# Performance work log

Measured on AMD Instinct MI355X. Metric: run time of the kernel, lower is better.

## Reference

```python
import jax, jax.numpy as jnp
import numpy as np

N_NODES = 50000
N_EDGES = 800000
NF = 128
HC = 128
NC = 40


def sage_conv(x, src, dst, Wl, Wr, b, num_nodes):
    """PyG SAGEConv with mean aggregation:
    out = lin_l(mean_{j in N(i)} x_j) + lin_r(x_i), bias folded into lin_l."""
    msgs = x[src]                                             # [E, F] gather
    agg = jax.ops.segment_sum(msgs, dst, num_segments=num_nodes)  # [N, F]
    cnt = jax.ops.segment_sum(jnp.ones((src.shape[0],), dtype=x.dtype), dst,
                              num_segments=num_nodes)          # [N]
    mean = agg / jnp.clip(cnt, 1.0)[:, None]                   # mean aggregation
    return mean @ Wl.T + x @ Wr.T + b


def setup_inputs() -> dict:
    key = jax.random.key(0)
    k = jax.random.split(key, 8)
    x = jax.random.normal(k[0], (N_NODES, NF), dtype=jnp.float32)
    edge_index = jax.random.randint(k[1], (2, N_EDGES), 0, N_NODES, dtype=jnp.int32)
    s1 = 1.0 / np.sqrt(NF)
    s2 = 1.0 / np.sqrt(HC)
    Wl1 = jax.random.uniform(k[2], (HC, NF), jnp.float32, -s1, s1)
    Wr1 = jax.random.uniform(k[3], (HC, NF), jnp.float32, -s1, s1)
    b1 = jnp.zeros((HC,), jnp.float32)
    Wl2 = jax.random.uniform(k[4], (NC, HC), jnp.float32, -s2, s2)
    Wr2 = jax.random.uniform(k[5], (NC, HC), jnp.float32, -s2, s2)
    b2 = jnp.zeros((NC,), jnp.float32)
    return {"x": x, "edge_index": edge_index, "Wl1": Wl1, "Wr1": Wr1,
            "b1": b1, "Wl2": Wl2, "Wr2": Wr2, "b2": b2}


def reference(x, edge_index, Wl1, Wr1, b1, Wl2, Wr2, b2):
    src, dst = edge_index[0], edge_index[1]
    num_nodes = x.shape[0]
    emb = sage_conv(x, src, dst, Wl1, Wr1, b1, num_nodes)      # embedding_output
    h = jax.nn.relu(emb)
    # F.dropout with training=False is the identity (inference reference)
    logits = sage_conv(h, src, dst, Wl2, Wr2, b2, num_nodes)
    return (logits, emb)
```

## Files before the change

kernel.cpp:

```cpp
#include <hip/hip_runtime.h>
#include <hip/hip_bf16.h>
#include <stdint.h>

#define NODES 50000
#define EDGES 800000
#define CAP   64

typedef __attribute__((ext_vector_type(8))) short bf16x8;
typedef __attribute__((ext_vector_type(8))) unsigned short u16x8;
typedef __attribute__((ext_vector_type(4))) float f32x4;
typedef unsigned short ushort_t;

__device__ __forceinline__ float4 ld4(const float* p) {
    return *reinterpret_cast<const float4*>(p);
}
__device__ __forceinline__ ushort_t f2bf(float f) {
    unsigned u = __float_as_uint(f);
    unsigned r = (u + 0x7fff + ((u >> 16) & 1)) >> 16;
    return (ushort_t)r;
}
__device__ __forceinline__ float bf2f(ushort_t h) {
    return __uint_as_float(((unsigned)h) << 16);
}

__global__ __launch_bounds__(256) void zerok(int* __restrict__ deg) {
    int t = blockIdx.x * 256 + threadIdx.x;
    if (t < 25000) reinterpret_cast<int2*>(deg)[t] = make_int2(0, 0);
}

__global__ __launch_bounds__(256) void prep(
    const float* __restrict__ x, const int* __restrict__ src,
    const int* __restrict__ dst,
    const float* __restrict__ Wr1, const float* __restrict__ Wl1,
    const float* __restrict__ Wr2, const float* __restrict__ Wl2,
    int* __restrict__ deg, ushort_t* __restrict__ esrc,
    ushort_t* __restrict__ A1, ushort_t* __restrict__ w1p,
    ushort_t* __restrict__ w2p) {
    int b = blockIdx.x;
    if (b < 3128) {
        int g = b & 7, chunk = b >> 3;
        int lo = g * 6250;
#pragma unroll
        for (int k = 0; k < 8; ++k) {
            int e = chunk * 2048 + k * 256 + threadIdx.x;
            if (e < EDGES) {
                int d = dst[e];
                if ((unsigned)(d - lo) < 6250u) {
                    int s = src[e];
                    int p = atomicAdd(&deg[d], 1);
                    if (p < CAP) esrc[(size_t)d * CAP + p] = (ushort_t)s;
                }
            }
        }
    } else if (b < 9378) {
        int idx = (b - 3128) * 256 + threadIdx.x;
        int i = idx >> 5, c = idx & 31;
        float4 v = ld4(x + (size_t)i * 128 + c * 4);
        ushort4 h;
        h.x = f2bf(v.x); h.y = f2bf(v.y); h.z = f2bf(v.z); h.w = f2bf(v.w);
        *reinterpret_cast<ushort4*>(A1 + (size_t)i * 256 + c * 4) = h;
    } else if (b < 9394) {
        int t = (b - 9378) * 256 + threadIdx.x;
        int nf = t >> 9, kc = (t >> 6) & 7, lane = t & 63;
        int r = nf * 16 + (lane & 15);
        int k2 = kc * 32 + ((lane >> 4) << 3);
        u16x8 o;
#pragma unroll
        for (int j = 0; j < 8; ++j) {
            int kk = k2 + j;
            float v = (kk < 128) ? Wr1[r * 128 + kk] : Wl1[r * 128 + (kk - 128)];
            o[j] = f2bf(v);
        }
        *reinterpret_cast<u16x8*>(w1p + (size_t)t * 8) = o;
    } else {
        int t = (b - 9394) * 256 + threadIdx.x;
        if (t >= 1280) return;
        int nf = t >> 8, kc = (t >> 6) & 3, lane = t & 63;
        int r = nf * 16 + (lane & 15);
        int k2 = kc * 32 + ((lane >> 4) << 3);
        u16x8 o;
#pragma unroll
        for (int j = 0; j < 8; ++j) {
            int kk = k2 + j;
            float v = (r < 40) ? Wr2[r * 128 + kk] : Wl2[(r - 40) * 128 + kk];
            o[j] = f2bf(v);
        }
        *reinterpret_cast<u16x8*>(w2p + (size_t)t * 8) = o;
    }
}

__global__ __launch_bounds__(256) void aggx(
    ushort_t* __restrict__ A1, const ushort_t* __restrict__ esrc,
    const int* __restrict__ deg) {
    int idx = blockIdx.x * 256 + threadIdx.x;
    int i = idx >> 4, c = idx & 15;
    int dg = deg[i];
    int n = dg < CAP ? dg : CAP;
    const ushort_t* ep = esrc + (size_t)i * CAP;
    float a0[8] = {}, a1[8] = {};
    int j = 0;
    for (; j + 8 <= n; j += 8) {
        int s0 = ep[j],     s1 = ep[j + 1], s2 = ep[j + 2], s3 = ep[j + 3];
        int s4 = ep[j + 4], s5 = ep[j + 5], s6 = ep[j + 6], s7 = ep[j + 7];
        u16x8 v0 = *reinterpret_cast<const u16x8*>(A1 + (size_t)s0 * 256 + c * 8);
        u16x8 v1 = *reinterpret_cast<const u16x8*>(A1 + (size_t)s1 * 256 + c * 8);
        u16x8 v2 = *reinterpret_cast<const u16x8*>(A1 + (size_t)s2 * 256 + c * 8);
        u16x8 v3 = *reinterpret_cast<const u16x8*>(A1 + (size_t)s3 * 256 + c * 8);
        u16x8 v4 = *reinterpret_cast<const u16x8*>(A1 + (size_t)s4 * 256 + c * 8);
        u16x8 v5 = *reinterpret_cast<const u16x8*>(A1 + (size_t)s5 * 256 + c * 8);
        u16x8 v6 = *reinterpret_cast<const u16x8*>(A1 + (size_t)s6 * 256 + c * 8);
        u16x8 v7 = *reinterpret_cast<const u16x8*>(A1 + (size_t)s7 * 256 + c * 8);
#pragma unroll
        for (int k = 0; k < 8; ++k) {
            a0[k] += (bf2f(v0[k]) + bf2f(v2[k])) + (bf2f(v4[k]) + bf2f(v6[k]));
            a1[k] += (bf2f(v1[k]) + bf2f(v3[k])) + (bf2f(v5[k]) + bf2f(v7[k]));
        }
    }
    for (; j + 4 <= n; j += 4) {
        int s0 = ep[j], s1 = ep[j + 1], s2 = ep[j + 2], s3 = ep[j + 3];
        u16x8 v0 = *reinterpret_cast<const u16x8*>(A1 + (size_t)s0 * 256 + c * 8);
        u16x8 v1 = *reinterpret_cast<const u16x8*>(A1 + (size_t)s1 * 256 + c * 8);
        u16x8 v2 = *reinterpret_cast<const u16x8*>(A1 + (size_t)s2 * 256 + c * 8);
        u16x8 v3 = *reinterpret_cast<const u16x8*>(A1 + (size_t)s3 * 256 + c * 8);
#pragma unroll
        for (int k = 0; k < 8; ++k) {
            a0[k] += bf2f(v0[k]) + bf2f(v2[k]);
            a1[k] += bf2f(v1[k]) + bf2f(v3[k]);
        }
    }
    for (; j < n; ++j) {
        int s = ep[j];
        u16x8 v = *reinterpret_cast<const u16x8*>(A1 + (size_t)s * 256 + c * 8);
#pragma unroll
        for (int k = 0; k < 8; ++k) a0[k] += bf2f(v[k]);
    }
    float ci = 1.0f / fmaxf((float)dg, 1.0f);
    u16x8 m;
#pragma unroll
    for (int k = 0; k < 8; ++k) m[k] = f2bf((a0[k] + a1[k]) * ci);
    *reinterpret_cast<u16x8*>(A1 + (size_t)i * 256 + 128 + c * 8) = m;
}

__global__ __launch_bounds__(256) void gemm12(
    const ushort_t* __restrict__ A1, const ushort_t* __restrict__ w1p,
    const ushort_t* __restrict__ w2p, const float* __restrict__ b1,
    float* __restrict__ emb, ushort_t* __restrict__ V, int M) {
    __shared__ ushort_t hs[64][136];
    const int wave = threadIdx.x >> 6, lane = threadIdx.x & 63;
    const int r0 = blockIdx.x * 64 + wave * 16;
    int arow = r0 + (lane & 15); if (arow >= M) arow = M - 1;
    const int klane = (lane >> 4) * 8;

    f32x4 acc[8] = {};
#pragma unroll
    for (int kc = 0; kc < 8; ++kc) {
        bf16x8 a = *reinterpret_cast<const bf16x8*>(A1 + (size_t)arow * 256 + kc * 32 + klane);
        bf16x8 wv[8];
#pragma unroll
        for (int nf = 0; nf < 8; ++nf)
            wv[nf] = *reinterpret_cast<const bf16x8*>(
                w1p + (size_t)((nf * 8 + kc) * 64 + lane) * 8);
#pragma unroll
        for (int nf = 0; nf < 8; ++nf)
            acc[nf] = __builtin_amdgcn_mfma_f32_16x16x32_bf16(a, wv[nf], acc[nf], 0, 0, 0);
    }

    const int crow0r = wave * 16 + (lane >> 4) * 4;
    const int crow0  = blockIdx.x * 64 + crow0r;
    const int ccol   = lane & 15;
#pragma unroll
    for (int nf = 0; nf < 8; ++nf) {
        int col = nf * 16 + ccol;
        float bv = b1[col];
#pragma unroll
        for (int r = 0; r < 4; ++r) {
            int row = crow0 + r;
            float val = acc[nf][r] + bv;
            if (row < M)
                __builtin_nontemporal_store(val, emb + (size_t)row * 128 + col);
            hs[crow0r + r][col] = f2bf(fmaxf(val, 0.f));
        }
    }
    __syncthreads();

    f32x4 acc2[5] = {};
#pragma unroll
    for (int kc = 0; kc < 4; ++kc) {
        bf16x8 a = *reinterpret_cast<const bf16x8*>(
            &hs[wave * 16 + (lane & 15)][kc * 32 + klane]);
        bf16x8 wv[5];
#pragma unroll
        for (int nf = 0; nf < 5; ++nf)
            wv[nf] = *reinterpret_cast<const bf16x8*>(
                w2p + (size_t)((nf * 4 + kc) * 64 + lane) * 8);
#pragma unroll
        for (int nf = 0; nf < 5; ++nf)
            acc2[nf] = __builtin_amdgcn_mfma_f32_16x16x32_bf16(a, wv[nf], acc2[nf], 0, 0, 0);
    }
#pragma unroll
    for (int nf = 0; nf < 5; ++nf) {
        int col = nf * 16 + ccol;
#pragma unroll
        for (int r = 0; r < 4; ++r) {
            int row = crow0 + r;
            if (row < M) V[(size_t)row * 80 + col] = f2bf(acc2[nf][r]);
        }
    }
}

__global__ __launch_bounds__(256) void agg2(
    const ushort_t* __restrict__ V, const ushort_t* __restrict__ esrc,
    const int* __restrict__ deg, const float* __restrict__ b2,
    float* __restrict__ logits) {
    int idx = blockIdx.x * 256 + threadIdx.x;
    int i = idx >> 3, c = idx & 7;
    if (i >= NODES || c >= 5) return;
    int dg = deg[i];
    int n = dg < CAP ? dg : CAP;
    const ushort_t* ep = esrc + (size_t)i * CAP;
    float a0[8] = {}, a1[8] = {};
    int j = 0;
    for (; j + 8 <= n; j += 8) {
        int s0 = ep[j],     s1 = ep[j + 1], s2 = ep[j + 2], s3 = ep[j + 3];
        int s4 = ep[j + 4], s5 = ep[j + 5], s6 = ep[j + 6], s7 = ep[j + 7];
        u16x8 v0 = *reinterpret_cast<const u16x8*>(V + (size_t)s0 * 80 + 40 + c * 8);
        u16x8 v1 = *reinterpret_cast<const u16x8*>(V + (size_t)s1 * 80 + 40 + c * 8);
        u16x8 v2 = *reinterpret_cast<const u16x8*>(V + (size_t)s2 * 80 + 40 + c * 8);
        u16x8 v3 = *reinterpret_cast<const u16x8*>(V + (size_t)s3 * 80 + 40 + c * 8);
        u16x8 v4 = *reinterpret_cast<const u16x8*>(V + (size_t)s4 * 80 + 40 + c * 8);
        u16x8 v5 = *reinterpret_cast<const u16x8*>(V + (size_t)s5 * 80 + 40 + c * 8);
        u16x8 v6 = *reinterpret_cast<const u16x8*>(V + (size_t)s6 * 80 + 40 + c * 8);
        u16x8 v7 = *reinterpret_cast<const u16x8*>(V + (size_t)s7 * 80 + 40 + c * 8);
#pragma unroll
        for (int k = 0; k < 8; ++k) {
            a0[k] += (bf2f(v0[k]) + bf2f(v2[k])) + (bf2f(v4[k]) + bf2f(v6[k]));
            a1[k] += (bf2f(v1[k]) + bf2f(v3[k])) + (bf2f(v5[k]) + bf2f(v7[k]));
        }
    }
    for (; j + 4 <= n; j += 4) {
        int s0 = ep[j], s1 = ep[j + 1], s2 = ep[j + 2], s3 = ep[j + 3];
        u16x8 v0 = *reinterpret_cast<const u16x8*>(V + (size_t)s0 * 80 + 40 + c * 8);
        u16x8 v1 = *reinterpret_cast<const u16x8*>(V + (size_t)s1 * 80 + 40 + c * 8);
        u16x8 v2 = *reinterpret_cast<const u16x8*>(V + (size_t)s2 * 80 + 40 + c * 8);
        u16x8 v3 = *reinterpret_cast<const u16x8*>(V + (size_t)s3 * 80 + 40 + c * 8);
#pragma unroll
        for (int k = 0; k < 8; ++k) {
            a0[k] += bf2f(v0[k]) + bf2f(v2[k]);
            a1[k] += bf2f(v1[k]) + bf2f(v3[k]);
        }
    }
    for (; j < n; ++j) {
        int s = ep[j];
        u16x8 v = *reinterpret_cast<const u16x8*>(V + (size_t)s * 80 + 40 + c * 8);
#pragma unroll
        for (int k = 0; k < 8; ++k) a0[k] += bf2f(v[k]);
    }
    float ci = 1.0f / fmaxf((float)dg, 1.0f);
    u16x8 sv = *reinterpret_cast<const u16x8*>(V + (size_t)i * 80 + c * 8);
    float o[8];
#pragma unroll
    for (int k = 0; k < 8; ++k)
        o[k] = bf2f(sv[k]) + (a0[k] + a1[k]) * ci + b2[c * 8 + k];
    float4* dst4 = reinterpret_cast<float4*>(logits + (size_t)i * 40 + c * 8);
    dst4[0] = make_float4(o[0], o[1], o[2], o[3]);
    dst4[1] = make_float4(o[4], o[5], o[6], o[7]);
}

extern "C" void kernel_launch(void* const* d_in, const int* in_sizes, int n_in,
                              void* d_out, int out_size, void* d_ws, size_t ws_size,
                              hipStream_t stream) {
    const float* x   = (const float*)d_in[0];
    const int*   ei  = (const int*)d_in[1];
    const float* Wl1 = (const float*)d_in[2];
    const float* Wr1 = (const float*)d_in[3];
    const float* b1  = (const float*)d_in[4];
    const float* Wl2 = (const float*)d_in[5];
    const float* Wr2 = (const float*)d_in[6];
    const float* b2  = (const float*)d_in[7];
    const int* src = ei;
    const int* dst = ei + EDGES;

    char* ws = (char*)d_ws;
    ushort_t* A1   = (ushort_t*)ws;
    ushort_t* V    = (ushort_t*)(ws + 25600000);
    ushort_t* esrc = (ushort_t*)(ws + 33600000);
    int*      deg  = (int*)(ws + 40000000);
    ushort_t* w1p  = (ushort_t*)(ws + 40200000);
    ushort_t* w2p  = (ushort_t*)(ws + 40265536);

    float* logits_out = (float*)d_out;
    float* emb_out    = logits_out + (size_t)NODES * 40;

    zerok<<<98, 256, 0, stream>>>(deg);

    prep<<<9399, 256, 0, stream>>>(x, src, dst, Wr1, Wl1, Wr2, Wl2,
                                   deg, esrc, A1, w1p, w2p);

    aggx<<<3125, 256, 0, stream>>>(A1, esrc, deg);

    gemm12<<<(NODES + 63) / 64, 256, 0, stream>>>(A1, w1p, w2p, b1, emb_out, V, NODES);

    agg2<<<(NODES * 8 + 255) / 256, 256, 0, stream>>>(V, esrc, deg, b2, logits_out);
}
```

Baseline: 119.4 us.

## Fuse layer-1 neighbor mean aggregation into the GEMM kernel via shared memory

The separate aggx kernel goes away. gemm12 now gathers and averages each 64-row tile's neighbor features into shared memory before running the MFMA GEMM. x in bf16 is stored in a compact 128-wide buffer instead of a 256-wide concatenated A1, so the mean half is never written to or re-read from global memory. This removes one launch and a round trip of the aggregated features. In exchange there is fewer-way parallelism per node in the gather (782 blocks, 4 rows per thread) and higher LDS use, which may reduce latency hiding during the irregular gather.

```diff
diff --git a/kernel.cpp b/kernel.cpp
--- a/kernel.cpp
+++ b/kernel.cpp
@@ -34,7 +34,7 @@
     const float* __restrict__ Wr1, const float* __restrict__ Wl1,
     const float* __restrict__ Wr2, const float* __restrict__ Wl2,
     int* __restrict__ deg, ushort_t* __restrict__ esrc,
-    ushort_t* __restrict__ A1, ushort_t* __restrict__ w1p,
+    ushort_t* __restrict__ xbf, ushort_t* __restrict__ w1p,
     ushort_t* __restrict__ w2p) {
     int b = blockIdx.x;
     if (b < 3128) {
@@ -58,7 +58,7 @@
         float4 v = ld4(x + (size_t)i * 128 + c * 4);
         ushort4 h;
         h.x = f2bf(v.x); h.y = f2bf(v.y); h.z = f2bf(v.z); h.w = f2bf(v.w);
-        *reinterpret_cast<ushort4*>(A1 + (size_t)i * 256 + c * 4) = h;
+        *reinterpret_cast<ushort4*>(xbf + (size_t)i * 128 + c * 4) = h;
     } else if (b < 9394) {
         int t = (b - 9378) * 256 + threadIdx.x;
         int nf = t >> 9, kc = (t >> 6) & 7, lane = t & 63;
@@ -89,72 +89,83 @@
     }
 }
 
-__global__ __launch_bounds__(256) void aggx(
-    ushort_t* __restrict__ A1, const ushort_t* __restrict__ esrc,
-    const int* __restrict__ deg) {
-    int idx = blockIdx.x * 256 + threadIdx.x;
-    int i = idx >> 4, c = idx & 15;
-    int dg = deg[i];
-    int n = dg < CAP ? dg : CAP;
-    const ushort_t* ep = esrc + (size_t)i * CAP;
-    float a0[8] = {}, a1[8] = {};
-    int j = 0;
-    for (; j + 8 <= n; j += 8) {
-        int s0 = ep[j],     s1 = ep[j + 1], s2 = ep[j + 2], s3 = ep[j + 3];
-        int s4 = ep[j + 4], s5 = ep[j + 5], s6 = ep[j + 6], s7 = ep[j + 7];
-        u16x8 v0 = *reinterpret_cast<const u16x8*>(A1 + (size_t)s0 * 256 + c * 8);
-        u16x8 v1 = *reinterpret_cast<const u16x8*>(A1 + (size_t)s1 * 256 + c * 8);
-        u16x8 v2 = *reinterpret_cast<const u16x8*>(A1 + (size_t)s2 * 256 + c * 8);
-        u16x8 v3 = *reinterpret_cast<const u16x8*>(A1 + (size_t)s3 * 256 + c * 8);
-        u16x8 v4 = *reinterpret_cast<const u16x8*>(A1 + (size_t)s4 * 256 + c * 8);
-        u16x8 v5 = *reinterpret_cast<const u16x8*>(A1 + (size_t)s5 * 256 + c * 8);
-        u16x8 v6 = *reinterpret_cast<const u16x8*>(A1 + (size_t)s6 * 256 + c * 8);
-        u16x8 v7 = *reinterpret_cast<const u16x8*>(A1 + (size_t)s7 * 256 + c * 8);
-#pragma unroll
-        for (int k = 0; k < 8; ++k) {
-            a0[k] += (bf2f(v0[k]) + bf2f(v2[k])) + (bf2f(v4[k]) + bf2f(v6[k]));
-            a1[k] += (bf2f(v1[k]) + bf2f(v3[k])) + (bf2f(v5[k]) + bf2f(v7[k]));
-        }
-    }
-    for (; j + 4 <= n; j += 4) {
-        int s0 = ep[j], s1 = ep[j + 1], s2 = ep[j + 2], s3 = ep[j + 3];
-        u16x8 v0 = *reinterpret_cast<const u16x8*>(A1 + (size_t)s0 * 256 + c * 8);
-        u16x8 v1 = *reinterpret_cast<const u16x8*>(A1 + (size_t)s1 * 256 + c * 8);
-        u16x8 v2 = *reinterpret_cast<const u16x8*>(A1 + (size_t)s2 * 256 + c * 8);
-        u16x8 v3 = *reinterpret_cast<const u16x8*>(A1 + (size_t)s3 * 256 + c * 8);
-#pragma unroll
-        for (int k = 0; k < 8; ++k) {
-            a0[k] += bf2f(v0[k]) + bf2f(v2[k]);
-            a1[k] += bf2f(v1[k]) + bf2f(v3[k]);
-        }
-    }
-    for (; j < n; ++j) {
-        int s = ep[j];
-        u16x8 v = *reinterpret_cast<const u16x8*>(A1 + (size_t)s * 256 + c * 8);
-#pragma unroll
-        for (int k = 0; k < 8; ++k) a0[k] += bf2f(v[k]);
-    }
-    float ci = 1.0f / fmaxf((float)dg, 1.0f);
-    u16x8 m;
-#pragma unroll
-    for (int k = 0; k < 8; ++k) m[k] = f2bf((a0[k] + a1[k]) * ci);
-    *reinterpret_cast<u16x8*>(A1 + (size_t)i * 256 + 128 + c * 8) = m;
-}
-
 __global__ __launch_bounds__(256) void gemm12(
-    const ushort_t* __restrict__ A1, const ushort_t* __restrict__ w1p,
+    const ushort_t* __restrict__ xbf, const ushort_t* __restrict__ esrc,
+    const int* __restrict__ deg, const ushort_t* __restrict__ w1p,
     const ushort_t* __restrict__ w2p, const float* __restrict__ b1,
     float* __restrict__ emb, ushort_t* __restrict__ V, int M) {
+    __shared__ ushort_t ms[64][136];
     __shared__ ushort_t hs[64][136];
-    const int wave = threadIdx.x >> 6, lane = threadIdx.x & 63;
-    const int r0 = blockIdx.x * 64 + wave * 16;
-    int arow = r0 + (lane & 15); if (arow >= M) arow = M - 1;
+    const int tid = threadIdx.x;
+    const int row0 = blockIdx.x * 64;
+
+    {
+        const int c = tid & 15, rloc = tid >> 4;
+#pragma unroll
+        for (int p = 0; p < 4; ++p) {
+            int rr = p * 16 + rloc;
+            int i = row0 + rr;
+            int dg = (i < M) ? deg[i] : 0;
+            int n = dg < CAP ? dg : CAP;
+            if (i >= M) n = 0;
+            const ushort_t* ep = esrc + (size_t)i * CAP;
+            float a0[8] = {}, a1[8] = {};
+            int j = 0;
+            for (; j + 8 <= n; j += 8) {
+                int s0 = ep[j],     s1 = ep[j + 1], s2 = ep[j + 2], s3 = ep[j + 3];
+                int s4 = ep[j + 4], s5 = ep[j + 5], s6 = ep[j + 6], s7 = ep[j + 7];
+                u16x8 v0 = *reinterpret_cast<const u16x8*>(xbf + (size_t)s0 * 128 + c * 8);
+                u16x8 v1 = *reinterpret_cast<const u16x8*>(xbf + (size_t)s1 * 128 + c * 8);
+                u16x8 v2 = *reinterpret_cast<const u16x8*>(xbf + (size_t)s2 * 128 + c * 8);
+                u16x8 v3 = *reinterpret_cast<const u16x8*>(xbf + (size_t)s3 * 128 + c * 8);
+                u16x8 v4 = *reinterpret_cast<const u16x8*>(xbf + (size_t)s4 * 128 + c * 8);
+                u16x8 v5 = *reinterpret_cast<const u16x8*>(xbf + (size_t)s5 * 128 + c * 8);
+                u16x8 v6 = *reinterpret_cast<const u16x8*>(xbf + (size_t)s6 * 128 + c * 8);
+                u16x8 v7 = *reinterpret_cast<const u16x8*>(xbf + (size_t)s7 * 128 + c * 8);
+#pragma unroll
+                for (int k = 0; k < 8; ++k) {
+                    a0[k] += (bf2f(v0[k]) + bf2f(v2[k])) + (bf2f(v4[k]) + bf2f(v6[k]));
+                    a1[k] += (bf2f(v1[k]) + bf2f(v3[k])) + (bf2f(v5[k]) + bf2f(v7[k]));
+                }
+            }
+            for (; j + 4 <= n; j += 4) {
+                int s0 = ep[j], s1 = ep[j + 1], s2 = ep[j + 2], s3 = ep[j + 3];
+                u16x8 v0 = *reinterpret_cast<const u16x8*>(xbf + (size_t)s0 * 128 + c * 8);
+                u16x8 v1 = *reinterpret_cast<const u16x8*>(xbf + (size_t)s1 * 128 + c * 8);
+                u16x8 v2 = *reinterpret_cast<const u16x8*>(xbf + (size_t)s2 * 128 + c * 8);
+                u16x8 v3 = *reinterpret_cast<const u16x8*>(xbf + (size_t)s3 * 128 + c * 8);
+#pragma unroll
+                for (int k = 0; k < 8; ++k) {
+                    a0[k] += bf2f(v0[k]) + bf2f(v2[k]);
+                    a1[k] += bf2f(v1[k]) + bf2f(v3[k]);
+                }
+            }
+            for (; j < n; ++j) {
+                int s = ep[j];
+                u16x8 v = *reinterpret_cast<const u16x8*>(xbf + (size_t)s * 128 + c * 8);
+#pragma unroll
+                for (int k = 0; k < 8; ++k) a0[k] += bf2f(v[k]);
+            }
+            float ci = 1.0f / fmaxf((float)dg, 1.0f);
+            u16x8 m;
+#pragma unroll
+            for (int k = 0; k < 8; ++k) m[k] = f2bf((a0[k] + a1[k]) * ci);
+            *reinterpret_cast<u16x8*>(&ms[rr][c * 8]) = m;
+        }
+    }
+    __syncthreads();
+
+    const int wave = tid >> 6, lane = tid & 63;
+    int arow = row0 + wave * 16 + (lane & 15); if (arow >= M) arow = M - 1;
+    const int rtile = wave * 16 + (lane & 15);
     const int klane = (lane >> 4) * 8;
 
     f32x4 acc[8] = {};
 #pragma unroll
     for (int kc = 0; kc < 8; ++kc) {
-        bf16x8 a = *reinterpret_cast<const bf16x8*>(A1 + (size_t)arow * 256 + kc * 32 + klane);
+        bf16x8 a = (kc < 4)
+            ? *reinterpret_cast<const bf16x8*>(xbf + (size_t)arow * 128 + kc * 32 + klane)
+            : *reinterpret_cast<const bf16x8*>(&ms[rtile][(kc - 4) * 32 + klane]);
         bf16x8 wv[8];
 #pragma unroll
         for (int nf = 0; nf < 8; ++nf)
@@ -166,7 +177,7 @@
     }
 
     const int crow0r = wave * 16 + (lane >> 4) * 4;
-    const int crow0  = blockIdx.x * 64 + crow0r;
+    const int crow0  = row0 + crow0r;
     const int ccol   = lane & 15;
 #pragma unroll
     for (int nf = 0; nf < 8; ++nf) {
@@ -186,8 +197,7 @@
     f32x4 acc2[5] = {};
 #pragma unroll
     for (int kc = 0; kc < 4; ++kc) {
-        bf16x8 a = *reinterpret_cast<const bf16x8*>(
-            &hs[wave * 16 + (lane & 15)][kc * 32 + klane]);
+        bf16x8 a = *reinterpret_cast<const bf16x8*>(&hs[rtile][kc * 32 + klane]);
         bf16x8 wv[5];
 #pragma unroll
         for (int nf = 0; nf < 5; ++nf)
@@ -281,12 +291,12 @@
     const int* dst = ei + EDGES;
 
     char* ws = (char*)d_ws;
-    ushort_t* A1   = (ushort_t*)ws;
-    ushort_t* V    = (ushort_t*)(ws + 25600000);
-    ushort_t* esrc = (ushort_t*)(ws + 33600000);
-    int*      deg  = (int*)(ws + 40000000);
-    ushort_t* w1p  = (ushort_t*)(ws + 40200000);
-    ushort_t* w2p  = (ushort_t*)(ws + 40265536);
+    ushort_t* xbf  = (ushort_t*)ws;
+    ushort_t* V    = (ushort_t*)(ws + 12800000);
+    ushort_t* esrc = (ushort_t*)(ws + 20800000);
+    int*      deg  = (int*)(ws + 27200000);
+    ushort_t* w1p  = (ushort_t*)(ws + 27400000);
+    ushort_t* w2p  = (ushort_t*)(ws + 27465536);
 
     float* logits_out = (float*)d_out;
     float* emb_out    = logits_out + (size_t)NODES * 40;
@@ -294,11 +304,10 @@
     zerok<<<98, 256, 0, stream>>>(deg);
 
     prep<<<9399, 256, 0, stream>>>(x, src, dst, Wr1, Wl1, Wr2, Wl2,
-                                   deg, esrc, A1, w1p, w2p);
-
-    aggx<<<3125, 256, 0, stream>>>(A1, esrc, deg);
-
-    gemm12<<<(NODES + 63) / 64, 256, 0, stream>>>(A1, w1p, w2p, b1, emb_out, V, NODES);
+                                   deg, esrc, xbf, w1p, w2p);
+
+    gemm12<<<(NODES + 63) / 64, 256, 0, stream>>>(xbf, esrc, deg, w1p, w2p, b1,
+                                                  emb_out, V, NODES);
 
     agg2<<<(NODES * 8 + 255) / 256, 256, 0, stream>>>(V, esrc, deg, b2, logits_out);
 }
```

Result: slower. 130.1 us (+9.0%).
